# Optimization experiments

Measured on AMD Instinct MI355X. Metric: run time of the kernel, lower is better.

## Reference

```python
import jax, jax.numpy as jnp
import numpy as np

INPUT_NDIMS = 1024
HIDDEN = 512
LATENT = 50
BATCH = 16384

def setup_inputs() -> dict:
    key = jax.random.key(0)
    ks = jax.random.split(key, 12)
    s = 0.02
    x = jax.random.uniform(ks[0], (BATCH, INPUT_NDIMS), dtype=jnp.float32)
    u = 0.01 + 0.98 * jax.random.uniform(ks[1], (BATCH, LATENT), dtype=jnp.float32)
    W1 = s * jax.random.normal(ks[2], (HIDDEN, INPUT_NDIMS), dtype=jnp.float32)
    b1 = jnp.zeros((HIDDEN,), jnp.float32)
    Wa = s * jax.random.normal(ks[3], (LATENT, HIDDEN), dtype=jnp.float32)
    ba = jnp.zeros((LATENT,), jnp.float32)
    Wb = s * jax.random.normal(ks[4], (LATENT, HIDDEN), dtype=jnp.float32)
    bb = jnp.zeros((LATENT,), jnp.float32)
    W2 = s * jax.random.normal(ks[5], (HIDDEN, LATENT), dtype=jnp.float32)
    b2 = jnp.zeros((HIDDEN,), jnp.float32)
    W3 = s * jax.random.normal(ks[6], (INPUT_NDIMS, HIDDEN), dtype=jnp.float32)
    b3 = jnp.zeros((INPUT_NDIMS,), jnp.float32)
    return dict(x=x, u=u, W1=W1, b1=b1, Wa=Wa, ba=ba, Wb=Wb, bb=bb, W2=W2, b2=b2, W3=W3, b3=b3)

def _stick_segments(v):
    # pi[:, k] = v[:, k] * prod_{j<k} (1 - v[:, j])  -- single O(K) cumprod pass
    cp = jnp.cumprod(1.0 - v, axis=1)                       # inclusive cumprod
    excl = jnp.concatenate([jnp.ones_like(cp[:, :1]), cp[:, :-1]], axis=1)
    return v * excl

def reference(x, u, W1, b1, Wa, ba, Wb, bb, W2, b2, W3, b3):
    # encoder: MLP -> positive Kumaraswamy params alpha (param1), beta (param2)
    h = jax.nn.relu(x @ W1.T + b1)                           # [B, H]
    alpha = jax.nn.softplus(h @ Wa.T + ba) + 1e-4            # [B, K]
    beta = jax.nn.softplus(h @ Wb.T + bb) + 1e-4             # [B, K]
    # Kumaraswamy reparameterized sample: v = (1 - u^(1/beta))^(1/alpha)
    v = jnp.power(1.0 - jnp.power(u, 1.0 / beta), 1.0 / alpha)
    # set_v_K_to_one: force last stick fraction to 1 so segments sum to 1
    v = v.at[:, -1].set(1.0)
    pi = _stick_segments(v)                                  # [B, K], rows sum to 1
    # decoder: MLP with sigmoid output
    h2 = jax.nn.relu(pi @ W2.T + b2)                         # [B, H]
    recon = jax.nn.sigmoid(h2 @ W3.T + b3)                   # [B, D]
    return recon, alpha, beta
```

## Files before the change

kernel.cpp:

```cpp
#include <hip/hip_runtime.h>
#include <hip/hip_bf16.h>

typedef __hip_bfloat16 bf16_t;
typedef __attribute__((ext_vector_type(4))) float f32x4;
typedef __attribute__((ext_vector_type(8))) __bf16 bf16x8;
typedef __attribute__((ext_vector_type(8))) short s16x8;
typedef __attribute__((ext_vector_type(4))) unsigned short u16x4;

#define BATCH 16384
#define NDIM  1024
#define HID   512
#define LAT   50

#define LOG2E 1.44269504088896340736f
#define RLOG2E 0.69314718055994530942f

__device__ __forceinline__ float ex2(float x) { return __builtin_amdgcn_exp2f(x); }
__device__ __forceinline__ float lg2(float x) { return __builtin_amdgcn_logf(x); }
__device__ __forceinline__ float rcp(float x) { return __builtin_amdgcn_rcpf(x); }

__device__ inline unsigned short f2b_u(float f) {
  union { bf16_t b; unsigned short u; } cv; cv.b = __float2bfloat16(f); return cv.u;
}

__device__ __forceinline__ void gload16(const void* src, void* dst_lds) {
  __builtin_amdgcn_global_load_lds(
      reinterpret_cast<const __attribute__((address_space(1))) void*>(
          reinterpret_cast<unsigned long long>(src)),
      reinterpret_cast<__attribute__((address_space(3))) void*>(
          static_cast<unsigned>(reinterpret_cast<unsigned long long>(dst_lds))),
      16, 0, 0);
}

#define WAIT_VMCNT(N)                                          \
  do {                                                         \
    asm volatile("s_waitcnt vmcnt(%0)" ::"i"(N) : "memory");   \
    __builtin_amdgcn_sched_barrier(0);                         \
  } while (0)

__global__ void prep_w_kernel(const float* __restrict__ W1, const float* __restrict__ W3,
                              const float* __restrict__ Wa, const float* __restrict__ Wb,
                              const float* __restrict__ W2, const float* __restrict__ ba,
                              const float* __restrict__ bb,
                              bf16_t* __restrict__ w1, bf16_t* __restrict__ w3,
                              bf16_t* __restrict__ wab, bf16_t* __restrict__ w2p,
                              float* __restrict__ bab)
{
  const int W1U  = (HID * NDIM) / 4;
  const int W3U  = (NDIM * HID) / 4;
  const int WABN = 128 * HID;
  const int W2PN = HID * 64;
  const int TOT  = W1U + W3U + WABN + W2PN + 128;
  for (int i = blockIdx.x * blockDim.x + threadIdx.x; i < TOT;
       i += gridDim.x * blockDim.x) {
    int j = i;
    if (j < W1U) {
      const f32x4 v = ((const f32x4*)W1)[j];
      u16x4 o; o[0]=f2b_u(v[0]); o[1]=f2b_u(v[1]); o[2]=f2b_u(v[2]); o[3]=f2b_u(v[3]);
      ((u16x4*)w1)[j] = o; continue;
    }
    j -= W1U;
    if (j < W3U) {
      const f32x4 v = ((const f32x4*)W3)[j];
      u16x4 o; o[0]=f2b_u(v[0]); o[1]=f2b_u(v[1]); o[2]=f2b_u(v[2]); o[3]=f2b_u(v[3]);
      ((u16x4*)w3)[j] = o; continue;
    }
    j -= W3U;
    if (j < WABN) {
      const int n = j >> 9, k = j & 511;
      float v = (n < 50) ? Wa[n * 512 + k] : ((n < 100) ? Wb[(n - 50) * 512 + k] : 0.f);
      wab[j] = __float2bfloat16(v); continue;
    }
    j -= WABN;
    if (j < W2PN) {
      const int n = j >> 6, k = j & 63;
      w2p[j] = __float2bfloat16(k < 50 ? W2[n * 50 + k] : 0.f); continue;
    }
    j -= W2PN;
    bab[j] = (j < 50) ? ba[j] : ((j < 100) ? bb[j - 50] : 0.f);
  }
}

template<int A_F32, int EPI, int MT, int NT>
__global__ __launch_bounds__(512, 4)
void gemm_kernel(const void* __restrict__ Av, const bf16_t* __restrict__ B,
                 const float* __restrict__ bias, void* __restrict__ out0,
                 int M, int N, int K)
{
  constexpr int MI  = MT / 32;
  constexpr int NI  = NT / 64;
  constexpr int IA  = MT / 64;
  constexpr int IB  = NT / 64;
  constexpr int L   = IA + IB;
  constexpr int BUF = MT * 128 + NT * 128;
  __shared__ char lds[2 * BUF];

  const int tid  = threadIdx.x;
  const int swzid = ((blockIdx.x & 7) * (gridDim.x >> 3)) + (blockIdx.x >> 3);
  const int nblocks = N / NT;
  const int bn   = swzid % nblocks;
  const int bm   = swzid / nblocks;
  const int wid  = tid >> 6;
  const int lane = tid & 63;
  const int l15  = lane & 15;
  const int l4   = lane >> 4;
  const int wm   = (wid >> 2) * (MT / 2);
  const int wn   = (wid & 3) * (NT / 4);
  const int uw   = __builtin_amdgcn_readfirstlane(wid);

  f32x4 acc[MI][NI] = {};
  f32x4 areg[2 * IA];

  auto stage_A = [&](char* buf, int k0) {
    const bf16_t* A = (const bf16_t*)Av;
    #pragma unroll
    for (int i = 0; i < IA; ++i) {
      const int c  = (i * 8 + uw) * 64 + lane;
      const int r  = c >> 3;
      const int sp = c & 7;
      const int sl = sp ^ (r & 7);
      gload16(A + (size_t)(bm * MT + r) * K + k0 + sl * 8,
              buf + (i * 8 + uw) * 1024);
    }
  };
  auto load_A_f32 = [&](int k0) {
    const float* A = (const float*)Av;
    #pragma unroll
    for (int i = 0; i < IA; ++i) {
      const int c  = i * 512 + tid;
      const int r  = c >> 3;
      const int sl = c & 7;
      const float* s = A + (size_t)(bm * MT + r) * K + k0 + sl * 8;
      areg[2 * i]     = *(const f32x4*)s;
      areg[2 * i + 1] = *(const f32x4*)(s + 4);
    }
  };
  auto write_A_f32 = [&](char* buf) {
    #pragma unroll
    for (int i = 0; i < IA; ++i) {
      const int c  = i * 512 + tid;
      const int r  = c >> 3;
      const int sl = c & 7;
      const int sp = sl ^ (r & 7);
      union { s16x8 v; unsigned short us[8]; } o;
      const f32x4 v0 = areg[2 * i], v1 = areg[2 * i + 1];
      o.us[0]=f2b_u(v0[0]); o.us[1]=f2b_u(v0[1]); o.us[2]=f2b_u(v0[2]); o.us[3]=f2b_u(v0[3]);
      o.us[4]=f2b_u(v1[0]); o.us[5]=f2b_u(v1[1]); o.us[6]=f2b_u(v1[2]); o.us[7]=f2b_u(v1[3]);
      *(s16x8*)(buf + r * 128 + sp * 16) = o.v;
    }
  };
  auto stage_B = [&](char* buf, int k0) {
    char* lB = buf + MT * 128;
    #pragma unroll
    for (int i = 0; i < IB; ++i) {
      const int c  = (i * 8 + uw) * 64 + lane;
      const int r  = c >> 3;
      const int sp = c & 7;
      const int sl = sp ^ (r & 7);
      gload16(B + (size_t)(bn * NT + r) * K + k0 + sl * 8,
              lB + (i * 8 + uw) * 1024);
    }
  };
  auto compute = [&](const char* buf) {
    const char* lA = buf;
    const char* lB = buf + MT * 128;
    #pragma unroll
    for (int h = 0; h < 2; ++h) {
      bf16x8 af[MI], bfr[NI];
      #pragma unroll
      for (int mi = 0; mi < MI; ++mi) {
        const int row = wm + mi * 16 + l15;
        const int sp  = (h * 4 + l4) ^ (row & 7);
        af[mi] = *(const bf16x8*)(lA + row * 128 + sp * 16);
      }
      #pragma unroll
      for (int ni = 0; ni < NI; ++ni) {
        const int row = wn + ni * 16 + l15;
        const int sp  = (h * 4 + l4) ^ (row & 7);
        bfr[ni] = *(const bf16x8*)(lB + row * 128 + sp * 16);
      }
      #pragma unroll
      for (int mi = 0; mi < MI; ++mi)
        #pragma unroll
        for (int ni = 0; ni < NI; ++ni)
          acc[mi][ni] = __builtin_amdgcn_mfma_f32_16x16x32_bf16(
              af[mi], bfr[ni], acc[mi][ni], 0, 0, 0);
    }
  };

  const int nt = K >> 6;
  if constexpr (A_F32) {
    load_A_f32(0); write_A_f32(lds); stage_B(lds, 0);
    __syncthreads();
    int cur = 0;
    for (int t = 0; t < nt - 1; ++t) {
      char* nbuf = lds + (cur ^ 1) * BUF;
      const int k0n = (t + 1) << 6;
      load_A_f32(k0n);
      stage_B(nbuf, k0n);
      compute(lds + cur * BUF);
      write_A_f32(nbuf);
      __syncthreads();
      cur ^= 1;
    }
    compute(lds + cur * BUF);
  } else {
    stage_A(lds, 0);      stage_B(lds, 0);
    if (nt > 1) { stage_A(lds + BUF, 64); stage_B(lds + BUF, 64); }
    for (int t = 0; t < nt; ++t) {
      if (t + 1 < nt) WAIT_VMCNT(L);
      else            WAIT_VMCNT(0);
      __builtin_amdgcn_s_barrier();
      compute(lds + (t & 1) * BUF);
      __builtin_amdgcn_s_barrier();
      __builtin_amdgcn_sched_barrier(0);
      if (t + 2 < nt) { stage_A(lds + (t & 1) * BUF, (t + 2) << 6);
                        stage_B(lds + (t & 1) * BUF, (t + 2) << 6); }
    }
  }

  #pragma unroll
  for (int ni = 0; ni < NI; ++ni) {
    const int n  = bn * NT + wn + ni * 16 + l15;
    const float bv = bias[n];
    #pragma unroll
    for (int mi = 0; mi < MI; ++mi) {
      #pragma unroll
      for (int r = 0; r < 4; ++r) {
        const int m  = bm * MT + wm + mi * 16 + l4 * 4 + r;
        const float t = acc[mi][ni][r] + bv;
        if (EPI == 0) {
          ((bf16_t*)out0)[(size_t)m * N + n] = __float2bfloat16(fmaxf(t, 0.f));
        } else {
          ((float*)out0)[(size_t)m * N + n] = rcp(1.f + ex2(-t * LOG2E));
        }
      }
    }
  }
}

__global__ __launch_bounds__(512, 2)
void abstick_kernel(const bf16_t* __restrict__ A, const bf16_t* __restrict__ wabg,
                    const float* __restrict__ bab, const bf16_t* __restrict__ w2pg,
                    const float* __restrict__ b2, const float* __restrict__ u,
                    float* __restrict__ out_a, float* __restrict__ out_b,
                    bf16_t* __restrict__ h2)
{
  constexpr int BUF = 64 * 128 + 16384;
  constexpr int PIL = 65536;
  constexpr int SMO = 73728;
  __shared__ char lds[100352];

  const int tid  = threadIdx.x;
  const int swzid = ((blockIdx.x & 7) * (gridDim.x >> 3)) + (blockIdx.x >> 3);
  const int bm   = swzid;
  const int wid  = tid >> 6;
  const int lane = tid & 63;
  const int l15  = lane & 15;
  const int l4   = lane >> 4;
  const int wm   = (wid >> 2) * 32;
  const int wn   = (wid & 3) * 32;
  const int uw   = __builtin_amdgcn_readfirstlane(wid);
  const int K    = HID;

  f32x4 acc[2][2] = {};

  auto stage_AB = [&](char* buf, int k0) {
    {
      const int c  = tid;
      const int r  = c >> 3;
      const int sp = c & 7;
      const int sl = sp ^ (r & 7);
      gload16(A + (size_t)(bm * 64 + r) * K + k0 + sl * 8, buf + uw * 1024);
    }
    char* lB = buf + 8192;
    #pragma unroll
    for (int i = 0; i < 2; ++i) {
      const int c  = (i * 8 + uw) * 64 + lane;
      const int r  = c >> 3;
      const int sp = c & 7;
      const int sl = sp ^ (r & 7);
      gload16(wabg + (size_t)r * K + k0 + sl * 8, lB + (i * 8 + uw) * 1024);
    }
  };
  auto compute1 = [&](const char* buf) {
    const char* lA = buf;
    const char* lB = buf + 8192;
    #pragma unroll
    for (int h = 0; h < 2; ++h) {
      bf16x8 af[2], bfr[2];
      #pragma unroll
      for (int mi = 0; mi < 2; ++mi) {
        const int row = wm + mi * 16 + l15;
        const int sp  = (h * 4 + l4) ^ (row & 7);
        af[mi] = *(const bf16x8*)(lA + row * 128 + sp * 16);
      }
      #pragma unroll
      for (int ni = 0; ni < 2; ++ni) {
        const int row = wn + ni * 16 + l15;
        const int sp  = (h * 4 + l4) ^ (row & 7);
        bfr[ni] = *(const bf16x8*)(lB + row * 128 + sp * 16);
      }
      #pragma unroll
      for (int mi = 0; mi < 2; ++mi)
        #pragma unroll
        for (int ni = 0; ni < 2; ++ni)
          acc[mi][ni] = __builtin_amdgcn_mfma_f32_16x16x32_bf16(
              af[mi], bfr[ni], acc[mi][ni], 0, 0, 0);
    }
  };

  stage_AB(lds, 0);
  stage_AB(lds + BUF, 64);
  for (int t = 0; t < 8; ++t) {
    if (t + 1 < 8) WAIT_VMCNT(3);
    else           WAIT_VMCNT(0);
    __builtin_amdgcn_s_barrier();
    compute1(lds + (t & 1) * BUF);
    __builtin_amdgcn_s_barrier();
    __builtin_amdgcn_sched_barrier(0);
    if (t + 2 < 8) stage_AB(lds + (t & 1) * BUF, (t + 2) << 6);
  }

  #pragma unroll
  for (int i = 0; i < 8; ++i) {
    const int c  = (i * 8 + uw) * 64 + lane;
    const int r  = c >> 3;
    const int sp = c & 7;
    const int sl = sp ^ (r & 7);
    gload16(w2pg + (size_t)r * 64 + sl * 8, lds + (i * 8 + uw) * 1024);
  }

  float* sm = (float*)(lds + SMO);
  #pragma unroll
  for (int ni = 0; ni < 2; ++ni) {
    const int n  = wn + ni * 16 + l15;
    const float bv = bab[n];
    #pragma unroll
    for (int mi = 0; mi < 2; ++mi) {
      #pragma unroll
      for (int r = 0; r < 4; ++r) {
        const int ml = wm + mi * 16 + l4 * 4 + r;
        const int m  = bm * 64 + ml;
        const float t = acc[mi][ni][r] + bv;
        if (n < 100) {
          const float y =
              (t > 20.f ? t : lg2(1.f + ex2(t * LOG2E)) * RLOG2E) + 1e-4f;
          if (n < 50) out_a[(size_t)m * 50 + n] = y;
          else        out_b[(size_t)m * 50 + (n - 50)] = y;
          sm[ml * 104 + n + (n < 50 ? 0 : 2)] = y;
        }
      }
    }
  }
  __syncthreads();

  #pragma unroll 1
  for (int rr = 0; rr < 8; ++rr) {
    const int rl = wid * 8 + rr;
    const size_t m = (size_t)(bm * 64 + rl);
    float v = 1.f, t = 1.f;
    if (lane < 49) {
      const float a  = sm[rl * 104 + lane];
      const float b  = sm[rl * 104 + 52 + lane];
      const float uu = u[m * 50 + lane];
      const float tb = ex2(lg2(uu) * rcp(b));
      v = ex2(lg2(1.f - tb) * rcp(a));
      t = 1.f - v;
    }
    float p = t;
    #pragma unroll
    for (int d = 1; d < 64; d <<= 1) {
      const float o = __shfl_up(p, d, 64);
      if (lane >= d) p *= o;
    }
    float e = __shfl_up(p, 1, 64);
    if (lane == 0) e = 1.f;
    const float piv = (lane < 50) ? v * e : 0.f;
    *(unsigned short*)(lds + PIL + rl * 128 +
                       (((lane >> 3) ^ (rl & 7)) << 4) + ((lane & 7) << 1)) =
        f2b_u(piv);
  }
  __syncthreads();

  const int wn3 = (wid & 3) * 128;
  f32x4 acc3[2][8] = {};
  #pragma unroll
  for (int h = 0; h < 2; ++h) {
    bf16x8 af[2], bfr[8];
    #pragma unroll
    for (int mi = 0; mi < 2; ++mi) {
      const int row = wm + mi * 16 + l15;
      const int sp  = (h * 4 + l4) ^ (row & 7);
      af[mi] = *(const bf16x8*)(lds + PIL + row * 128 + sp * 16);
    }
    #pragma unroll
    for (int ni = 0; ni < 8; ++ni) {
      const int row = wn3 + ni * 16 + l15;
      const int sp  = (h * 4 + l4) ^ (row & 7);
      bfr[ni] = *(const bf16x8*)(lds + row * 128 + sp * 16);
    }
    #pragma unroll
    for (int mi = 0; mi < 2; ++mi)
      #pragma unroll
      for (int ni = 0; ni < 8; ++ni)
        acc3[mi][ni] = __builtin_amdgcn_mfma_f32_16x16x32_bf16(
            af[mi], bfr[ni], acc3[mi][ni], 0, 0, 0);
  }
  #pragma unroll
  for (int ni = 0; ni < 8; ++ni) {
    const int n  = wn3 + ni * 16 + l15;
    const float bv = b2[n];
    #pragma unroll
    for (int mi = 0; mi < 2; ++mi) {
      #pragma unroll
      for (int r = 0; r < 4; ++r) {
        const int m  = bm * 64 + wm + mi * 16 + l4 * 4 + r;
        h2[(size_t)m * HID + n] =
            __float2bfloat16(fmaxf(acc3[mi][ni][r] + bv, 0.f));
      }
    }
  }
}

extern "C" void kernel_launch(void* const* d_in, const int* in_sizes, int n_in,
                              void* d_out, int out_size, void* d_ws, size_t ws_size,
                              hipStream_t stream)
{
  const float* x  = (const float*)d_in[0];
  const float* u  = (const float*)d_in[1];
  const float* W1 = (const float*)d_in[2];
  const float* b1 = (const float*)d_in[3];
  const float* Wa = (const float*)d_in[4];
  const float* ba = (const float*)d_in[5];
  const float* Wb = (const float*)d_in[6];
  const float* bb = (const float*)d_in[7];
  const float* W2 = (const float*)d_in[8];
  const float* b2 = (const float*)d_in[9];
  const float* W3 = (const float*)d_in[10];
  const float* b3 = (const float*)d_in[11];

  float* recon  = (float*)d_out;
  float* oalpha = recon + (size_t)BATCH * NDIM;
  float* obeta  = oalpha + (size_t)BATCH * LAT;

  char* ws = (char*)d_ws;
  bf16_t* h2  = (bf16_t*)(ws);
  bf16_t* h   = (bf16_t*)(ws + 16777216);
  bf16_t* w1  = (bf16_t*)(ws + 33554432);
  bf16_t* w3  = (bf16_t*)(ws + 34603008);
  bf16_t* wab = (bf16_t*)(ws + 35651584);
  bf16_t* w2p = (bf16_t*)(ws + 35782656);
  float*  bab = (float*)(ws + 35848192);

  prep_w_kernel<<<512, 256, 0, stream>>>(W1, W3, Wa, Wb, W2, ba, bb,
                                         w1, w3, wab, w2p, bab);
  gemm_kernel<1, 0, 64, 256><<<512, 512, 0, stream>>>(
      x, w1, b1, (void*)h, BATCH, HID, NDIM);
  abstick_kernel<<<256, 512, 0, stream>>>(
      h, wab, bab, w2p, b2, u, oalpha, obeta, h2);
  gemm_kernel<0, 1, 64, 256><<<1024, 512, 0, stream>>>(
      h2, w3, b3, (void*)recon, BATCH, NDIM, HID);
}
```

Baseline: 80.59 us.

## Use larger GEMM tiles with interleaved prefetch and per-quarter MFMA scheduling

```diff
diff --git a/kernel.cpp b/kernel.cpp
--- a/kernel.cpp
+++ b/kernel.cpp
@@ -35,6 +35,11 @@
 #define WAIT_VMCNT(N)                                          \
   do {                                                         \
     asm volatile("s_waitcnt vmcnt(%0)" ::"i"(N) : "memory");   \
+    __builtin_amdgcn_sched_barrier(0);                         \
+  } while (0)
+#define WAIT_LGKM0                                             \
+  do {                                                         \
+    asm volatile("s_waitcnt lgkmcnt(0)" ::: "memory");         \
     __builtin_amdgcn_sched_barrier(0);                         \
   } while (0)
 
@@ -81,153 +86,160 @@
   }
 }
 
-template<int A_F32, int EPI, int MT, int NT>
-__global__ __launch_bounds__(512, 4)
-void gemm_kernel(const void* __restrict__ Av, const bf16_t* __restrict__ B,
-                 const float* __restrict__ bias, void* __restrict__ out0,
-                 int M, int N, int K)
+template<int A_F32, int EPI, int BM>
+__global__ __launch_bounds__(512, 2)
+void gemm256_kernel(const void* __restrict__ Av, const bf16_t* __restrict__ B,
+                    const float* __restrict__ bias, void* __restrict__ out0,
+                    int M, int N, int K)
 {
-  constexpr int MI  = MT / 32;
-  constexpr int NI  = NT / 64;
-  constexpr int IA  = MT / 64;
-  constexpr int IB  = NT / 64;
-  constexpr int L   = IA + IB;
-  constexpr int BUF = MT * 128 + NT * 128;
+  constexpr int BN  = 256;
+  constexpr int BUF = (BM + BN) * 128;
+  constexpr int RA  = BM / 64;
+  constexpr int MI  = BM / 32;
+  constexpr int FPQ = MI / 4;
   __shared__ char lds[2 * BUF];
 
   const int tid  = threadIdx.x;
   const int swzid = ((blockIdx.x & 7) * (gridDim.x >> 3)) + (blockIdx.x >> 3);
-  const int nblocks = N / NT;
+  const int nblocks = N / BN;
   const int bn   = swzid % nblocks;
   const int bm   = swzid / nblocks;
   const int wid  = tid >> 6;
   const int lane = tid & 63;
   const int l15  = lane & 15;
   const int l4   = lane >> 4;
-  const int wm   = (wid >> 2) * (MT / 2);
-  const int wn   = (wid & 3) * (NT / 4);
+  const int wm   = (wid >> 2) * (BM / 2);
+  const int wn   = (wid & 3) * 64;
   const int uw   = __builtin_amdgcn_readfirstlane(wid);
 
-  f32x4 acc[MI][NI] = {};
-  f32x4 areg[2 * IA];
-
-  auto stage_A = [&](char* buf, int k0) {
+  f32x4 acc[MI][4] = {};
+  f32x4 areg[4];
+
+  auto stage_A_round = [&](char* buf, int k0, int i) {
     const bf16_t* A = (const bf16_t*)Av;
-    #pragma unroll
-    for (int i = 0; i < IA; ++i) {
-      const int c  = (i * 8 + uw) * 64 + lane;
-      const int r  = c >> 3;
-      const int sp = c & 7;
-      const int sl = sp ^ (r & 7);
-      gload16(A + (size_t)(bm * MT + r) * K + k0 + sl * 8,
-              buf + (i * 8 + uw) * 1024);
-    }
+    const int c  = (i * 8 + uw) * 64 + lane;
+    const int r  = c >> 3;
+    const int sp = c & 7;
+    const int sl = sp ^ (r & 7);
+    gload16(A + (size_t)(bm * BM + r) * K + k0 + sl * 8,
+            buf + (i * 8 + uw) * 1024);
+  };
+  auto stage_B_round = [&](char* buf, int k0, int i) {
+    char* lB = buf + BM * 128;
+    const int c  = (i * 8 + uw) * 64 + lane;
+    const int r  = c >> 3;
+    const int sp = c & 7;
+    const int sl = sp ^ (r & 7);
+    gload16(B + (size_t)(bn * BN + r) * K + k0 + sl * 8,
+            lB + (i * 8 + uw) * 1024);
   };
   auto load_A_f32 = [&](int k0) {
     const float* A = (const float*)Av;
     #pragma unroll
-    for (int i = 0; i < IA; ++i) {
-      const int c  = i * 512 + tid;
+    for (int j = 0; j < 2; ++j) {
+      const int c  = j * 512 + tid;
       const int r  = c >> 3;
       const int sl = c & 7;
-      const float* s = A + (size_t)(bm * MT + r) * K + k0 + sl * 8;
-      areg[2 * i]     = *(const f32x4*)s;
-      areg[2 * i + 1] = *(const f32x4*)(s + 4);
+      const float* s = A + (size_t)(bm * BM + r) * K + k0 + sl * 8;
+      areg[2 * j]     = *(const f32x4*)s;
+      areg[2 * j + 1] = *(const f32x4*)(s + 4);
     }
   };
   auto write_A_f32 = [&](char* buf) {
     #pragma unroll
-    for (int i = 0; i < IA; ++i) {
-      const int c  = i * 512 + tid;
+    for (int j = 0; j < 2; ++j) {
+      const int c  = j * 512 + tid;
       const int r  = c >> 3;
       const int sl = c & 7;
       const int sp = sl ^ (r & 7);
       union { s16x8 v; unsigned short us[8]; } o;
-      const f32x4 v0 = areg[2 * i], v1 = areg[2 * i + 1];
+      const f32x4 v0 = areg[2 * j], v1 = areg[2 * j + 1];
       o.us[0]=f2b_u(v0[0]); o.us[1]=f2b_u(v0[1]); o.us[2]=f2b_u(v0[2]); o.us[3]=f2b_u(v0[3]);
       o.us[4]=f2b_u(v1[0]); o.us[5]=f2b_u(v1[1]); o.us[6]=f2b_u(v1[2]); o.us[7]=f2b_u(v1[3]);
       *(s16x8*)(buf + r * 128 + sp * 16) = o.v;
     }
   };
-  auto stage_B = [&](char* buf, int k0) {
-    char* lB = buf + MT * 128;
-    #pragma unroll
-    for (int i = 0; i < IB; ++i) {
-      const int c  = (i * 8 + uw) * 64 + lane;
-      const int r  = c >> 3;
-      const int sp = c & 7;
-      const int sl = sp ^ (r & 7);
-      gload16(B + (size_t)(bn * NT + r) * K + k0 + sl * 8,
-              lB + (i * 8 + uw) * 1024);
-    }
-  };
-  auto compute = [&](const char* buf) {
+
+  const int nt = K >> 6;
+  if constexpr (A_F32) {
+    load_A_f32(0); write_A_f32(lds);
+  } else {
+    #pragma unroll
+    for (int i = 0; i < RA; ++i) stage_A_round(lds, 0, i);
+  }
+  #pragma unroll
+  for (int i = 0; i < 4; ++i) stage_B_round(lds, 0, i);
+  WAIT_VMCNT(0);
+  WAIT_LGKM0;
+  __builtin_amdgcn_s_barrier();
+
+  for (int t = 0; t < nt; ++t) {
+    char* buf  = lds + (t & 1) * BUF;
+    char* nbuf = lds + ((t + 1) & 1) * BUF;
     const char* lA = buf;
-    const char* lB = buf + MT * 128;
-    #pragma unroll
-    for (int h = 0; h < 2; ++h) {
-      bf16x8 af[MI], bfr[NI];
-      #pragma unroll
-      for (int mi = 0; mi < MI; ++mi) {
-        const int row = wm + mi * 16 + l15;
-        const int sp  = (h * 4 + l4) ^ (row & 7);
-        af[mi] = *(const bf16x8*)(lA + row * 128 + sp * 16);
-      }
-      #pragma unroll
-      for (int ni = 0; ni < NI; ++ni) {
+    const char* lB = buf + BM * 128;
+    const bool pf  = (t + 1 < nt);
+    const int k0n  = (t + 1) << 6;
+
+    if (A_F32 && pf) load_A_f32(k0n);
+
+    bf16x8 bfr[4][2];
+    #pragma unroll
+    for (int ni = 0; ni < 4; ++ni)
+      #pragma unroll
+      for (int h = 0; h < 2; ++h) {
         const int row = wn + ni * 16 + l15;
         const int sp  = (h * 4 + l4) ^ (row & 7);
-        bfr[ni] = *(const bf16x8*)(lB + row * 128 + sp * 16);
-      }
-      #pragma unroll
-      for (int mi = 0; mi < MI; ++mi)
+        bfr[ni][h] = *(const bf16x8*)(lB + row * 128 + sp * 16);
+      }
+
+    #pragma unroll
+    for (int q = 0; q < 4; ++q) {
+      if (pf) {
+        if constexpr (A_F32) {
+          stage_B_round(nbuf, k0n, q);
+        } else {
+          if (q < RA) stage_A_round(nbuf, k0n, q);
+          stage_B_round(nbuf, k0n, q);
+        }
+      }
+      bf16x8 af[FPQ][2];
+      #pragma unroll
+      for (int f = 0; f < FPQ; ++f)
         #pragma unroll
-        for (int ni = 0; ni < NI; ++ni)
-          acc[mi][ni] = __builtin_amdgcn_mfma_f32_16x16x32_bf16(
-              af[mi], bfr[ni], acc[mi][ni], 0, 0, 0);
-    }
-  };
-
-  const int nt = K >> 6;
-  if constexpr (A_F32) {
-    load_A_f32(0); write_A_f32(lds); stage_B(lds, 0);
-    __syncthreads();
-    int cur = 0;
-    for (int t = 0; t < nt - 1; ++t) {
-      char* nbuf = lds + (cur ^ 1) * BUF;
-      const int k0n = (t + 1) << 6;
-      load_A_f32(k0n);
-      stage_B(nbuf, k0n);
-      compute(lds + cur * BUF);
-      write_A_f32(nbuf);
-      __syncthreads();
-      cur ^= 1;
-    }
-    compute(lds + cur * BUF);
-  } else {
-    stage_A(lds, 0);      stage_B(lds, 0);
-    if (nt > 1) { stage_A(lds + BUF, 64); stage_B(lds + BUF, 64); }
-    for (int t = 0; t < nt; ++t) {
-      if (t + 1 < nt) WAIT_VMCNT(L);
-      else            WAIT_VMCNT(0);
-      __builtin_amdgcn_s_barrier();
-      compute(lds + (t & 1) * BUF);
-      __builtin_amdgcn_s_barrier();
-      __builtin_amdgcn_sched_barrier(0);
-      if (t + 2 < nt) { stage_A(lds + (t & 1) * BUF, (t + 2) << 6);
-                        stage_B(lds + (t & 1) * BUF, (t + 2) << 6); }
-    }
-  }
-
-  #pragma unroll
-  for (int ni = 0; ni < NI; ++ni) {
-    const int n  = bn * NT + wn + ni * 16 + l15;
+        for (int h = 0; h < 2; ++h) {
+          const int row = wm + (q * FPQ + f) * 16 + l15;
+          const int sp  = (h * 4 + l4) ^ (row & 7);
+          af[f][h] = *(const bf16x8*)(lA + row * 128 + sp * 16);
+        }
+      WAIT_LGKM0;
+      __builtin_amdgcn_s_setprio(1);
+      #pragma unroll
+      for (int f = 0; f < FPQ; ++f)
+        #pragma unroll
+        for (int ni = 0; ni < 4; ++ni)
+          #pragma unroll
+          for (int h = 0; h < 2; ++h)
+            acc[q * FPQ + f][ni] = __builtin_amdgcn_mfma_f32_16x16x32_bf16(
+                af[f][h], bfr[ni][h], acc[q * FPQ + f][ni], 0, 0, 0);
+      __builtin_amdgcn_s_setprio(0);
+    }
+
+    if (A_F32 && pf) write_A_f32(nbuf);
+    WAIT_VMCNT(0);
+    WAIT_LGKM0;
+    __builtin_amdgcn_s_barrier();
+  }
+
+  #pragma unroll
+  for (int ni = 0; ni < 4; ++ni) {
+    const int n  = bn * BN + wn + ni * 16 + l15;
     const float bv = bias[n];
     #pragma unroll
     for (int mi = 0; mi < MI; ++mi) {
       #pragma unroll
       for (int r = 0; r < 4; ++r) {
-        const int m  = bm * MT + wm + mi * 16 + l4 * 4 + r;
+        const int m  = bm * BM + wm + mi * 16 + l4 * 4 + r;
         const float t = acc[mi][ni][r] + bv;
         if (EPI == 0) {
           ((bf16_t*)out0)[(size_t)m * N + n] = __float2bfloat16(fmaxf(t, 0.f));
@@ -455,10 +467,10 @@
 
   prep_w_kernel<<<512, 256, 0, stream>>>(W1, W3, Wa, Wb, W2, ba, bb,
                                          w1, w3, wab, w2p, bab);
-  gemm_kernel<1, 0, 64, 256><<<512, 512, 0, stream>>>(
+  gemm256_kernel<1, 0, 128><<<256, 512, 0, stream>>>(
       x, w1, b1, (void*)h, BATCH, HID, NDIM);
   abstick_kernel<<<256, 512, 0, stream>>>(
       h, wab, bab, w2p, b2, u, oalpha, obeta, h2);
-  gemm_kernel<0, 1, 64, 256><<<1024, 512, 0, stream>>>(
+  gemm256_kernel<0, 1, 256><<<256, 512, 0, stream>>>(
       h2, w3, b3, (void*)recon, BATCH, NDIM, HID);
 }
```

Result: no change. 79.55 us (-1.3%).
